# Kernel tuning notes

Hardware: AMD Instinct MI355X
Metric: run time of the kernel (lower is better)

The kernel has to match this reference:

```python
import jax, jax.numpy as jnp
import numpy as np

D_MODEL = 1024
NUM_HEADS = 16
D_K = D_MODEL // NUM_HEADS


def setup_inputs() -> dict:
    key = jax.random.key(0)
    ks = jax.random.split(key, 9)
    B, S = 2, 2048
    s_in = 1.0 / np.sqrt(D_MODEL)
    x = jax.random.normal(ks[0], (B, S, D_MODEL), dtype=jnp.float32)
    # Linear weights stored as (in_features, out_features): y = x @ W + b
    Wq = jax.random.uniform(ks[1], (D_MODEL, D_MODEL), jnp.float32, -s_in, s_in)
    bq = jax.random.uniform(ks[2], (D_MODEL,), jnp.float32, -s_in, s_in)
    Wk = jax.random.uniform(ks[3], (D_MODEL, D_K), jnp.float32, -s_in, s_in)
    bk = jax.random.uniform(ks[4], (D_K,), jnp.float32, -s_in, s_in)
    Wv = jax.random.uniform(ks[5], (D_MODEL, D_K), jnp.float32, -s_in, s_in)
    bv = jax.random.uniform(ks[6], (D_K,), jnp.float32, -s_in, s_in)
    Wo = jax.random.uniform(ks[7], (D_MODEL, D_MODEL), jnp.float32, -s_in, s_in)
    bo = jax.random.uniform(ks[8], (D_MODEL,), jnp.float32, -s_in, s_in)
    return {"x": x, "Wq": Wq, "bq": bq, "Wk": Wk, "bk": bk,
            "Wv": Wv, "bv": bv, "Wo": Wo, "bo": bo}


def reference(x, Wq, bq, Wk, bk, Wv, bv, Wo, bo):
    B, S, _ = x.shape
    H, Dk = NUM_HEADS, D_K
    # Projections
    Q = (x @ Wq + bq).reshape(B, S, H, Dk).transpose(0, 2, 1, 3)  # [B,H,S,Dk]
    K = x @ Wk + bk                                               # [B,S,Dk] single KV head
    V = x @ Wv + bv                                               # [B,S,Dk]
    # Scores: query heads broadcast against the single shared KV head
    scores = jnp.einsum('bhqd,bkd->bhqk', Q, K) / jnp.sqrt(jnp.float32(Dk))
    attn = jax.nn.softmax(scores, axis=-1)                        # [B,H,S,S]
    out = jnp.einsum('bhqk,bkd->bhqd', attn, V)                   # [B,H,S,Dk]
    out = out.transpose(0, 2, 1, 3).reshape(B, S, H * Dk)         # [B,S,d_model]
    return out @ Wo + bo
```

## Files before the change

### kernel.cpp

```cpp
#include <hip/hip_runtime.h>
#include <hip/hip_bf16.h>

typedef __attribute__((ext_vector_type(8))) short bf16x8;
typedef __attribute__((ext_vector_type(4))) float f32x4;
typedef __attribute__((ext_vector_type(16))) float f32x16;
typedef __attribute__((ext_vector_type(4))) unsigned short ushort4v;

#define QSCALE 0.1803368801111204f

__device__ __forceinline__ unsigned short f2bf(float f) {
  union { float f; unsigned int u; } x; x.f = f;
  unsigned int u = x.u;
  unsigned int r = (u + 0x7fffu + ((u >> 16) & 1u)) >> 16;
  return (unsigned short)r;
}

__device__ __forceinline__ unsigned int bfpack2(float a, float b) {
  union { __hip_bfloat162 h; unsigned int u; } c;
  c.h = __float22bfloat162_rn(make_float2(a, b));
  return c.u;
}

__global__ __launch_bounds__(256) void prep_kernel(
    const float* __restrict__ x,
    const float* __restrict__ Wq, const float* __restrict__ Wk,
    const float* __restrict__ Wv, const float* __restrict__ Wo,
    unsigned short* __restrict__ xb,
    unsigned short* __restrict__ QKVt, unsigned short* __restrict__ Wot) {
  int z = blockIdx.z;
  if (z == 4) {
    size_t base = ((size_t)(blockIdx.y * 32 + blockIdx.x)) * 4096 + threadIdx.x * 16;
#pragma unroll
    for (int c = 0; c < 4; ++c) {
      float4 v = *(const float4*)(x + base + c * 4);
      ushort4v o = { f2bf(v.x), f2bf(v.y), f2bf(v.z), f2bf(v.w) };
      *(ushort4v*)(xb + base + c * 4) = o;
    }
    return;
  }
  __shared__ float t[32][33];
  const float* src;
  unsigned short* dst;
  int C, rowoff;
  if (z == 0)      { src = Wq; dst = QKVt; C = 1024; rowoff = 0; }
  else if (z == 1) { src = Wk; dst = QKVt; C = 64;   rowoff = 1024; }
  else if (z == 2) { src = Wv; dst = QKVt; C = 64;   rowoff = 1088; }
  else             { src = Wo; dst = Wot;  C = 1024; rowoff = 0; }
  int c0 = blockIdx.x * 32, r0 = blockIdx.y * 32;
  if (c0 >= C) return;
  int tx = threadIdx.x & 31, ty = threadIdx.x >> 5;
#pragma unroll
  for (int i = 0; i < 32; i += 8)
    t[ty + i][tx] = src[(size_t)(r0 + ty + i) * C + c0 + tx];
  __syncthreads();
#pragma unroll
  for (int i = 0; i < 32; i += 8)
    dst[(size_t)(rowoff + c0 + ty + i) * 1024 + r0 + tx] = f2bf(t[tx][ty + i]);
}

template <typename OutT, bool QKVMODE>
__global__ __launch_bounds__(256) void gemm_bf16_kernel(
    const unsigned short* __restrict__ A, const unsigned short* __restrict__ Bt,
    const float* __restrict__ b0, const float* __restrict__ b1,
    const float* __restrict__ b2, OutT* __restrict__ C,
    unsigned short* __restrict__ Vt, int M, int N, int K) {
  constexpr int LS = 40;
  __shared__ unsigned short As[2][128 * LS];
  __shared__ unsigned short Bs[2][128 * LS];
  int tid = threadIdx.x;
  int wid = tid >> 6, lane = tid & 63;
  int l15 = lane & 15, quad = lane >> 4;
  int m0 = blockIdx.x * 128, n0 = blockIdx.y * 128;
  int mw = (wid >> 1) * 64, nw = (wid & 1) * 64;
  f32x4 acc[4][4];
#pragma unroll
  for (int i = 0; i < 4; i++)
#pragma unroll
    for (int j = 0; j < 4; j++)
#pragma unroll
      for (int e = 0; e < 4; ++e) acc[i][j][e] = 0.f;

  int arow = tid >> 2, akc = (tid & 3) * 8;
  const unsigned short* Ag = A + (size_t)(m0 + arow) * K + akc;
  const unsigned short* Bg = Bt + (size_t)(n0 + arow) * K + akc;
  bf16x8 ar0 = *(const bf16x8*)(Ag);
  bf16x8 ar1 = *(const bf16x8*)(Ag + (size_t)64 * K);
  bf16x8 br0 = *(const bf16x8*)(Bg);
  bf16x8 br1 = *(const bf16x8*)(Bg + (size_t)64 * K);

  for (int k0 = 0; k0 < K; k0 += 32) {
    unsigned short* Asb = As[(k0 >> 5) & 1];
    unsigned short* Bsb = Bs[(k0 >> 5) & 1];
    *(bf16x8*)(Asb + arow * LS + akc) = ar0;
    *(bf16x8*)(Asb + (arow + 64) * LS + akc) = ar1;
    *(bf16x8*)(Bsb + arow * LS + akc) = br0;
    *(bf16x8*)(Bsb + (arow + 64) * LS + akc) = br1;
    __syncthreads();
    if (k0 + 32 < K) {
      ar0 = *(const bf16x8*)(Ag + k0 + 32);
      ar1 = *(const bf16x8*)(Ag + (size_t)64 * K + k0 + 32);
      br0 = *(const bf16x8*)(Bg + k0 + 32);
      br1 = *(const bf16x8*)(Bg + (size_t)64 * K + k0 + 32);
    }
    bf16x8 af[4], bfr[4];
#pragma unroll
    for (int t = 0; t < 4; ++t)
      af[t] = *(const bf16x8*)(Asb + (mw + t * 16 + l15) * LS + quad * 8);
#pragma unroll
    for (int t = 0; t < 4; ++t)
      bfr[t] = *(const bf16x8*)(Bsb + (nw + t * 16 + l15) * LS + quad * 8);
#pragma unroll
    for (int mt = 0; mt < 4; ++mt)
#pragma unroll
      for (int nt = 0; nt < 4; ++nt)
        acc[mt][nt] = __builtin_amdgcn_mfma_f32_16x16x32_bf16(
            af[mt], bfr[nt], acc[mt][nt], 0, 0, 0);
  }
#pragma unroll
  for (int mt = 0; mt < 4; ++mt)
#pragma unroll
    for (int nt = 0; nt < 4; ++nt) {
      int col = n0 + nw + nt * 16 + l15;
      float bias, cs;
      if constexpr (QKVMODE) {
        bias = (col < 1024) ? b0[col] : ((col < 1088) ? b1[col - 1024] : b2[col - 1088]);
        cs = (col < 1024) ? QSCALE : 1.0f;
      } else {
        bias = b0[col];
        cs = 1.0f;
      }
#pragma unroll
      for (int r = 0; r < 4; ++r) {
        int row = m0 + mw + mt * 16 + quad * 4 + r;
        float v = (acc[mt][nt][r] + bias) * cs;
        if constexpr (sizeof(OutT) == 2)
          C[(size_t)row * N + col] = f2bf(v);
        else
          C[(size_t)row * N + col] = v;
        if constexpr (QKVMODE) {
          if (col >= 1088)
            Vt[((size_t)(row >> 11) * 64 + (col - 1088)) * 2048 + (row & 2047)] =
                f2bf(v);
        }
      }
    }
}

__global__ __launch_bounds__(256) void flash_attn_kernel(
    const unsigned short* __restrict__ QKV,
    const unsigned short* __restrict__ Vt,
    unsigned short* __restrict__ AO) {
  constexpr int S = 2048, LDQ = 1152;
  constexpr int PK = 72;
  __shared__ unsigned short Ks[2][64 * PK];
  __shared__ unsigned short Vs[2][64 * PK];
  int tid = threadIdx.x;
  int wid = tid >> 6, lane = tid & 63;
  int l31 = lane & 31, half = lane >> 5;
  int q0 = blockIdx.x * 128, h = blockIdx.y, b = blockIdx.z;

  const unsigned short* Qb =
      QKV + (size_t)(b * S + q0 + wid * 32 + l31) * LDQ + h * 64 + half * 8;
  bf16x8 qf[4];
#pragma unroll
  for (int f = 0; f < 4; ++f) qf[f] = *(const bf16x8*)(Qb + f * 16);

  int srow = tid >> 3, skc = (tid & 7) * 8;
  const unsigned short* Kg = QKV + ((size_t)(b * S + srow) * LDQ + 1024 + skc);
  const unsigned short* Vg = Vt + ((size_t)(b * 64 + srow) * 2048 + skc);

  f32x16 oacc[2];
#pragma unroll
  for (int r = 0; r < 16; ++r) { oacc[0][r] = 0.f; oacc[1][r] = 0.f; }
  float rsacc = 0.f;

  bf16x8 kr0 = *(const bf16x8*)(Kg);
  bf16x8 kr1 = *(const bf16x8*)(Kg + (size_t)32 * LDQ);
  bf16x8 vr0 = *(const bf16x8*)(Vg);
  bf16x8 vr1 = *(const bf16x8*)(Vg + (size_t)32 * 2048);

  for (int kb = 0; kb < S; kb += 64) {
    unsigned short* Ksb = Ks[(kb >> 6) & 1];
    unsigned short* Vsb = Vs[(kb >> 6) & 1];
    *(bf16x8*)(Ksb + srow * PK + skc) = kr0;
    *(bf16x8*)(Ksb + (srow + 32) * PK + skc) = kr1;
    *(bf16x8*)(Vsb + srow * PK + skc) = vr0;
    *(bf16x8*)(Vsb + (srow + 32) * PK + skc) = vr1;
    __syncthreads();
    if (kb + 64 < S) {
      kr0 = *(const bf16x8*)(Kg + (size_t)(kb + 64) * LDQ);
      kr1 = *(const bf16x8*)(Kg + (size_t)(kb + 96) * LDQ);
      vr0 = *(const bf16x8*)(Vg + kb + 64);
      vr1 = *(const bf16x8*)(Vg + (size_t)32 * 2048 + kb + 64);
    }

    unsigned int pk[2][8];
#pragma unroll
    for (int n2 = 0; n2 < 2; ++n2) {
      f32x16 sacc;
#pragma unroll
      for (int i = 0; i < 16; ++i) sacc[i] = 0.f;
#pragma unroll
      for (int s4 = 0; s4 < 4; ++s4) {
        bf16x8 kf = *(const bf16x8*)(Ksb + (n2 * 32 + l31) * PK + s4 * 16 + half * 8);
        sacc = __builtin_amdgcn_mfma_f32_32x32x16_bf16(kf, qf[s4], sacc, 0, 0, 0);
      }
#pragma unroll
      for (int v = 0; v < 8; ++v) {
        float p0 = __builtin_amdgcn_exp2f(sacc[2 * v]);
        float p1 = __builtin_amdgcn_exp2f(sacc[2 * v + 1]);
        rsacc += p0 + p1;
        pk[n2][v] = bfpack2(p0, p1);
      }
    }
    unsigned int other[2][8];
#pragma unroll
    for (int n2 = 0; n2 < 2; ++n2)
#pragma unroll
      for (int v = 0; v < 8; ++v) other[n2][v] = __shfl_xor(pk[n2][v], 32);

    bf16x8 pfr[4];
#pragma unroll
    for (int s = 0; s < 4; ++s) {
      int n2 = s >> 1, vb = 4 * (s & 1);
      union { bf16x8 v; unsigned int u[4]; } fr;
      fr.u[0] = half ? other[n2][vb + 2] : pk[n2][vb + 0];
      fr.u[1] = half ? other[n2][vb + 3] : pk[n2][vb + 1];
      fr.u[2] = half ? pk[n2][vb + 2]    : other[n2][vb + 0];
      fr.u[3] = half ? pk[n2][vb + 3]    : other[n2][vb + 1];
      pfr[s] = fr.v;
    }

#pragma unroll
    for (int d2 = 0; d2 < 2; ++d2)
#pragma unroll
      for (int s = 0; s < 4; ++s) {
        bf16x8 vf = *(const bf16x8*)(Vsb + (d2 * 32 + l31) * PK + s * 16 + half * 8);
        oacc[d2] = __builtin_amdgcn_mfma_f32_32x32x16_bf16(vf, pfr[s], oacc[d2], 0, 0, 0);
      }
  }

  float inv = 1.0f / (rsacc + __shfl_xor(rsacc, 32));

  unsigned short* Ob = AO + (size_t)(b * S + q0 + wid * 32 + l31) * 1024 + h * 64;
#pragma unroll
  for (int d2 = 0; d2 < 2; ++d2)
#pragma unroll
    for (int g = 0; g < 4; ++g) {
      union { ushort4v s4; unsigned int u[2]; } w;
      w.u[0] = bfpack2(oacc[d2][4 * g + 0] * inv, oacc[d2][4 * g + 1] * inv);
      w.u[1] = bfpack2(oacc[d2][4 * g + 2] * inv, oacc[d2][4 * g + 3] * inv);
      *(ushort4v*)(Ob + d2 * 32 + 8 * g + 4 * half) = w.s4;
    }
}

extern "C" void kernel_launch(void* const* d_in, const int* in_sizes, int n_in,
                              void* d_out, int out_size, void* d_ws, size_t ws_size,
                              hipStream_t stream) {
  const float* x  = (const float*)d_in[0];
  const float* Wq = (const float*)d_in[1];
  const float* bq = (const float*)d_in[2];
  const float* Wk = (const float*)d_in[3];
  const float* bk = (const float*)d_in[4];
  const float* Wv = (const float*)d_in[5];
  const float* bv = (const float*)d_in[6];
  const float* Wo = (const float*)d_in[7];
  const float* bo = (const float*)d_in[8];
  float* out = (float*)d_out;

  constexpr int B = 2, S = 2048, D = 1024, Dk = 64, H = 16;
  constexpr int M = B * S;
  constexpr int NQKV = D + 2 * Dk;

  char* ws = (char*)d_ws;
  unsigned short* xb   = (unsigned short*)ws; ws += (size_t)M * D * 2;
  unsigned short* QKVt = (unsigned short*)ws; ws += (size_t)NQKV * D * 2;
  unsigned short* Wot  = (unsigned short*)ws; ws += (size_t)D * D * 2;
  unsigned short* QKV  = (unsigned short*)ws; ws += (size_t)M * NQKV * 2;
  unsigned short* Vtb  = (unsigned short*)ws; ws += (size_t)B * Dk * S * 2;
  unsigned short* AO   = (unsigned short*)ws; ws += (size_t)M * D * 2;

  prep_kernel<<<dim3(32, 32, 5), 256, 0, stream>>>(x, Wq, Wk, Wv, Wo, xb, QKVt, Wot);

  gemm_bf16_kernel<unsigned short, true><<<dim3(M / 128, NQKV / 128), 256, 0, stream>>>(
      xb, QKVt, bq, bk, bv, QKV, Vtb, M, NQKV, D);

  flash_attn_kernel<<<dim3(S / 128, H, B), 256, 0, stream>>>(QKV, Vtb, AO);

  gemm_bf16_kernel<float, false><<<dim3(M / 128, D / 128), 256, 0, stream>>>(
      AO, Wot, bo, nullptr, nullptr, out, nullptr, M, D, D);
}
```

Before: 194.3 us.

## Shrink GEMM N-tile to 64 and rework attention around 16x16 MFMA tiles

The GEMM kernel now uses 128x64 tiles instead of 128x128, which doubles the number of blocks for the QKV and output projections and raises parallelism across CUs. The attention kernel is rewritten to give each wave 16 query rows using 16x16x32 MFMA instead of 32x32x16. The P fragments are now rearranged with ds_bpermute, and the launch bound now requests 4 blocks per CU. This is meant to improve occupancy and load balance, since the old grids had few blocks. In exchange, the smaller tiles lower per-block data reuse and add more redundant K/V loads into LDS.

```diff
diff --git a/kernel.cpp b/kernel.cpp
--- a/kernel.cpp
+++ b/kernel.cpp
@@ -3,7 +3,6 @@
 
 typedef __attribute__((ext_vector_type(8))) short bf16x8;
 typedef __attribute__((ext_vector_type(4))) float f32x4;
-typedef __attribute__((ext_vector_type(16))) float f32x16;
 typedef __attribute__((ext_vector_type(4))) unsigned short ushort4v;
 
 #define QSCALE 0.1803368801111204f
@@ -15,8 +14,8 @@
   return (unsigned short)r;
 }
 
-__device__ __forceinline__ unsigned int bfpack2(float a, float b) {
-  union { __hip_bfloat162 h; unsigned int u; } c;
+__device__ __forceinline__ int bfpack2(float a, float b) {
+  union { __hip_bfloat162 h; int u; } c;
   c.h = __float22bfloat162_rn(make_float2(a, b));
   return c.u;
 }
@@ -66,27 +65,26 @@
     unsigned short* __restrict__ Vt, int M, int N, int K) {
   constexpr int LS = 40;
   __shared__ unsigned short As[2][128 * LS];
-  __shared__ unsigned short Bs[2][128 * LS];
+  __shared__ unsigned short Bs[2][64 * LS];
   int tid = threadIdx.x;
   int wid = tid >> 6, lane = tid & 63;
   int l15 = lane & 15, quad = lane >> 4;
-  int m0 = blockIdx.x * 128, n0 = blockIdx.y * 128;
-  int mw = (wid >> 1) * 64, nw = (wid & 1) * 64;
-  f32x4 acc[4][4];
+  int m0 = blockIdx.x * 128, n0 = blockIdx.y * 64;
+  int mw = (wid >> 1) * 64, nw = (wid & 1) * 32;
+  f32x4 acc[4][2];
 #pragma unroll
   for (int i = 0; i < 4; i++)
 #pragma unroll
-    for (int j = 0; j < 4; j++)
+    for (int j = 0; j < 2; j++)
 #pragma unroll
       for (int e = 0; e < 4; ++e) acc[i][j][e] = 0.f;
 
   int arow = tid >> 2, akc = (tid & 3) * 8;
   const unsigned short* Ag = A + (size_t)(m0 + arow) * K + akc;
-  const unsigned short* Bg = Bt + (size_t)(n0 + arow) * K + akc;
+  const unsigned short* Bg = Bt + (size_t)(n0 + (tid >> 2)) * K + akc;
   bf16x8 ar0 = *(const bf16x8*)(Ag);
   bf16x8 ar1 = *(const bf16x8*)(Ag + (size_t)64 * K);
   bf16x8 br0 = *(const bf16x8*)(Bg);
-  bf16x8 br1 = *(const bf16x8*)(Bg + (size_t)64 * K);
 
   for (int k0 = 0; k0 < K; k0 += 32) {
     unsigned short* Asb = As[(k0 >> 5) & 1];
@@ -94,32 +92,30 @@
     *(bf16x8*)(Asb + arow * LS + akc) = ar0;
     *(bf16x8*)(Asb + (arow + 64) * LS + akc) = ar1;
     *(bf16x8*)(Bsb + arow * LS + akc) = br0;
-    *(bf16x8*)(Bsb + (arow + 64) * LS + akc) = br1;
     __syncthreads();
     if (k0 + 32 < K) {
       ar0 = *(const bf16x8*)(Ag + k0 + 32);
       ar1 = *(const bf16x8*)(Ag + (size_t)64 * K + k0 + 32);
       br0 = *(const bf16x8*)(Bg + k0 + 32);
-      br1 = *(const bf16x8*)(Bg + (size_t)64 * K + k0 + 32);
-    }
-    bf16x8 af[4], bfr[4];
+    }
+    bf16x8 af[4], bfr[2];
 #pragma unroll
     for (int t = 0; t < 4; ++t)
       af[t] = *(const bf16x8*)(Asb + (mw + t * 16 + l15) * LS + quad * 8);
 #pragma unroll
-    for (int t = 0; t < 4; ++t)
+    for (int t = 0; t < 2; ++t)
       bfr[t] = *(const bf16x8*)(Bsb + (nw + t * 16 + l15) * LS + quad * 8);
 #pragma unroll
     for (int mt = 0; mt < 4; ++mt)
 #pragma unroll
-      for (int nt = 0; nt < 4; ++nt)
+      for (int nt = 0; nt < 2; ++nt)
         acc[mt][nt] = __builtin_amdgcn_mfma_f32_16x16x32_bf16(
             af[mt], bfr[nt], acc[mt][nt], 0, 0, 0);
   }
 #pragma unroll
   for (int mt = 0; mt < 4; ++mt)
 #pragma unroll
-    for (int nt = 0; nt < 4; ++nt) {
+    for (int nt = 0; nt < 2; ++nt) {
       int col = n0 + nw + nt * 16 + l15;
       float bias, cs;
       if constexpr (QKVMODE) {
@@ -146,7 +142,7 @@
     }
 }
 
-__global__ __launch_bounds__(256) void flash_attn_kernel(
+__global__ __launch_bounds__(256, 4) void flash_attn_kernel(
     const unsigned short* __restrict__ QKV,
     const unsigned short* __restrict__ Vt,
     unsigned short* __restrict__ AO) {
@@ -156,22 +152,28 @@
   __shared__ unsigned short Vs[2][64 * PK];
   int tid = threadIdx.x;
   int wid = tid >> 6, lane = tid & 63;
-  int l31 = lane & 31, half = lane >> 5;
-  int q0 = blockIdx.x * 128, h = blockIdx.y, b = blockIdx.z;
+  int l15 = lane & 15, quad = lane >> 4;
+  int q0 = blockIdx.x * 64, h = blockIdx.y, b = blockIdx.z;
 
   const unsigned short* Qb =
-      QKV + (size_t)(b * S + q0 + wid * 32 + l31) * LDQ + h * 64 + half * 8;
-  bf16x8 qf[4];
-#pragma unroll
-  for (int f = 0; f < 4; ++f) qf[f] = *(const bf16x8*)(Qb + f * 16);
+      QKV + (size_t)(b * S + q0 + wid * 16 + l15) * LDQ + h * 64 + quad * 8;
+  bf16x8 qf[2];
+  qf[0] = *(const bf16x8*)(Qb);
+  qf[1] = *(const bf16x8*)(Qb + 32);
 
   int srow = tid >> 3, skc = (tid & 7) * 8;
   const unsigned short* Kg = QKV + ((size_t)(b * S + srow) * LDQ + 1024 + skc);
   const unsigned short* Vg = Vt + ((size_t)(b * 64 + srow) * 2048 + skc);
 
-  f32x16 oacc[2];
-#pragma unroll
-  for (int r = 0; r < 16; ++r) { oacc[0][r] = 0.f; oacc[1][r] = 0.f; }
+  int addrA = ((((quad << 1)) & 3) * 16 + l15) << 2;
+  int addrB = ((((quad << 1) + 1) & 3) * 16 + l15) << 2;
+  bool hi = quad >= 2;
+
+  f32x4 oacc[4];
+#pragma unroll
+  for (int i = 0; i < 4; ++i)
+#pragma unroll
+    for (int e = 0; e < 4; ++e) oacc[i][e] = 0.f;
   float rsacc = 0.f;
 
   bf16x8 kr0 = *(const bf16x8*)(Kg);
@@ -194,64 +196,69 @@
       vr1 = *(const bf16x8*)(Vg + (size_t)32 * 2048 + kb + 64);
     }
 
-    unsigned int pk[2][8];
-#pragma unroll
-    for (int n2 = 0; n2 < 2; ++n2) {
-      f32x16 sacc;
-#pragma unroll
-      for (int i = 0; i < 16; ++i) sacc[i] = 0.f;
-#pragma unroll
-      for (int s4 = 0; s4 < 4; ++s4) {
-        bf16x8 kf = *(const bf16x8*)(Ksb + (n2 * 32 + l31) * PK + s4 * 16 + half * 8);
-        sacc = __builtin_amdgcn_mfma_f32_32x32x16_bf16(kf, qf[s4], sacc, 0, 0, 0);
-      }
-#pragma unroll
-      for (int v = 0; v < 8; ++v) {
-        float p0 = __builtin_amdgcn_exp2f(sacc[2 * v]);
-        float p1 = __builtin_amdgcn_exp2f(sacc[2 * v + 1]);
-        rsacc += p0 + p1;
-        pk[n2][v] = bfpack2(p0, p1);
-      }
-    }
-    unsigned int other[2][8];
-#pragma unroll
-    for (int n2 = 0; n2 < 2; ++n2)
-#pragma unroll
-      for (int v = 0; v < 8; ++v) other[n2][v] = __shfl_xor(pk[n2][v], 32);
-
-    bf16x8 pfr[4];
-#pragma unroll
-    for (int s = 0; s < 4; ++s) {
-      int n2 = s >> 1, vb = 4 * (s & 1);
-      union { bf16x8 v; unsigned int u[4]; } fr;
-      fr.u[0] = half ? other[n2][vb + 2] : pk[n2][vb + 0];
-      fr.u[1] = half ? other[n2][vb + 3] : pk[n2][vb + 1];
-      fr.u[2] = half ? pk[n2][vb + 2]    : other[n2][vb + 0];
-      fr.u[3] = half ? pk[n2][vb + 3]    : other[n2][vb + 1];
-      pfr[s] = fr.v;
-    }
-
-#pragma unroll
-    for (int d2 = 0; d2 < 2; ++d2)
-#pragma unroll
-      for (int s = 0; s < 4; ++s) {
-        bf16x8 vf = *(const bf16x8*)(Vsb + (d2 * 32 + l31) * PK + s * 16 + half * 8);
-        oacc[d2] = __builtin_amdgcn_mfma_f32_32x32x16_bf16(vf, pfr[s], oacc[d2], 0, 0, 0);
-      }
-  }
-
-  float inv = 1.0f / (rsacc + __shfl_xor(rsacc, 32));
-
-  unsigned short* Ob = AO + (size_t)(b * S + q0 + wid * 32 + l31) * 1024 + h * 64;
-#pragma unroll
-  for (int d2 = 0; d2 < 2; ++d2)
-#pragma unroll
-    for (int g = 0; g < 4; ++g) {
-      union { ushort4v s4; unsigned int u[2]; } w;
-      w.u[0] = bfpack2(oacc[d2][4 * g + 0] * inv, oacc[d2][4 * g + 1] * inv);
-      w.u[1] = bfpack2(oacc[d2][4 * g + 2] * inv, oacc[d2][4 * g + 3] * inv);
-      *(ushort4v*)(Ob + d2 * 32 + 8 * g + 4 * half) = w.s4;
-    }
+    f32x4 sacc[4];
+#pragma unroll
+    for (int mt = 0; mt < 4; ++mt)
+#pragma unroll
+      for (int e = 0; e < 4; ++e) sacc[mt][e] = 0.f;
+#pragma unroll
+    for (int mt = 0; mt < 4; ++mt)
+#pragma unroll
+      for (int c = 0; c < 2; ++c) {
+        bf16x8 kf =
+            *(const bf16x8*)(Ksb + (mt * 16 + l15) * PK + c * 32 + quad * 8);
+        sacc[mt] = __builtin_amdgcn_mfma_f32_16x16x32_bf16(kf, qf[c], sacc[mt], 0, 0, 0);
+      }
+
+    int held[4][2];
+#pragma unroll
+    for (int mt = 0; mt < 4; ++mt) {
+      float p0 = __builtin_amdgcn_exp2f(sacc[mt][0]);
+      float p1 = __builtin_amdgcn_exp2f(sacc[mt][1]);
+      float p2 = __builtin_amdgcn_exp2f(sacc[mt][2]);
+      float p3 = __builtin_amdgcn_exp2f(sacc[mt][3]);
+      rsacc += (p0 + p1) + (p2 + p3);
+      held[mt][0] = bfpack2(p0, p1);
+      held[mt][1] = bfpack2(p2, p3);
+    }
+
+    bf16x8 pfr[2];
+#pragma unroll
+    for (int c = 0; c < 2; ++c) {
+      union { bf16x8 v; int u[4]; } fr;
+#pragma unroll
+      for (int d2 = 0; d2 < 4; ++d2) {
+        int a = (d2 & 2) ? addrB : addrA;
+        int t0 = __builtin_amdgcn_ds_bpermute(a, held[2 * c][d2 & 1]);
+        int t1 = __builtin_amdgcn_ds_bpermute(a, held[2 * c + 1][d2 & 1]);
+        fr.u[d2] = hi ? t1 : t0;
+      }
+      pfr[c] = fr.v;
+    }
+
+#pragma unroll
+    for (int mt2 = 0; mt2 < 4; ++mt2)
+#pragma unroll
+      for (int c = 0; c < 2; ++c) {
+        bf16x8 vf =
+            *(const bf16x8*)(Vsb + (mt2 * 16 + l15) * PK + c * 32 + quad * 8);
+        oacc[mt2] = __builtin_amdgcn_mfma_f32_16x16x32_bf16(vf, pfr[c], oacc[mt2], 0, 0, 0);
+      }
+  }
+
+  float s = rsacc;
+  s += __shfl_xor(s, 16);
+  s += __shfl_xor(s, 32);
+  float inv = 1.0f / s;
+
+  unsigned short* Ob = AO + (size_t)(b * S + q0 + wid * 16 + l15) * 1024 + h * 64;
+#pragma unroll
+  for (int mt2 = 0; mt2 < 4; ++mt2) {
+    union { ushort4v s4; int u[2]; } w;
+    w.u[0] = bfpack2(oacc[mt2][0] * inv, oacc[mt2][1] * inv);
+    w.u[1] = bfpack2(oacc[mt2][2] * inv, oacc[mt2][3] * inv);
+    *(ushort4v*)(Ob + mt2 * 16 + quad * 4) = w.s4;
+  }
 }
 
 extern "C" void kernel_launch(void* const* d_in, const int* in_sizes, int n_in,
@@ -282,11 +289,11 @@
 
   prep_kernel<<<dim3(32, 32, 5), 256, 0, stream>>>(x, Wq, Wk, Wv, Wo, xb, QKVt, Wot);
 
-  gemm_bf16_kernel<unsigned short, true><<<dim3(M / 128, NQKV / 128), 256, 0, stream>>>(
+  gemm_bf16_kernel<unsigned short, true><<<dim3(M / 128, NQKV / 64), 256, 0, stream>>>(
       xb, QKVt, bq, bk, bv, QKV, Vtb, M, NQKV, D);
 
-  flash_attn_kernel<<<dim3(S / 128, H, B), 256, 0, stream>>>(QKV, Vtb, AO);
-
-  gemm_bf16_kernel<float, false><<<dim3(M / 128, D / 128), 256, 0, stream>>>(
+  flash_attn_kernel<<<dim3(S / 64, H, B), 256, 0, stream>>>(QKV, Vtb, AO);
+
+  gemm_bf16_kernel<float, false><<<dim3(M / 128, D / 64), 256, 0, stream>>>(
       AO, Wot, bo, nullptr, nullptr, out, nullptr, M, D, D);
 }
```

New measurement: 203.1 us. 1.05x slower.

## Fuse x bf16 conversion into QKV GEMM, shrink GEMM N-tile, stage P via LDS

Applied to the files above, without the earlier changes.

Drops the separate x fp32-to-bf16 pass: the QKV GEMM now loads fp32 x directly and packs it to bf16 while staging into shared memory, which removes one full read and write of the activation buffer. Both GEMMs switch to 128x64 tiles, doubling the block count for better CU occupancy at the cost of less data reuse per block. The attention kernel now writes the P matrix to a per-wave LDS buffer and reads it back as the MFMA operand, replacing the cross-lane shuffles and selects. That adds LDS traffic and a write-then-read dependency on shared memory.

```diff
diff --git a/kernel.cpp b/kernel.cpp
--- a/kernel.cpp
+++ b/kernel.cpp
@@ -15,30 +15,27 @@
   return (unsigned short)r;
 }
 
-__device__ __forceinline__ unsigned int bfpack2(float a, float b) {
-  union { __hip_bfloat162 h; unsigned int u; } c;
+__device__ __forceinline__ int bfpack2(float a, float b) {
+  union { __hip_bfloat162 h; int u; } c;
   c.h = __float22bfloat162_rn(make_float2(a, b));
   return c.u;
 }
 
+__device__ __forceinline__ bf16x8 pack8(float4 a, float4 b) {
+  union { bf16x8 v; int u[4]; } c;
+  c.u[0] = bfpack2(a.x, a.y);
+  c.u[1] = bfpack2(a.z, a.w);
+  c.u[2] = bfpack2(b.x, b.y);
+  c.u[3] = bfpack2(b.z, b.w);
+  return c.v;
+}
+
 __global__ __launch_bounds__(256) void prep_kernel(
-    const float* __restrict__ x,
     const float* __restrict__ Wq, const float* __restrict__ Wk,
     const float* __restrict__ Wv, const float* __restrict__ Wo,
-    unsigned short* __restrict__ xb,
     unsigned short* __restrict__ QKVt, unsigned short* __restrict__ Wot) {
+  __shared__ float t[32][33];
   int z = blockIdx.z;
-  if (z == 4) {
-    size_t base = ((size_t)(blockIdx.y * 32 + blockIdx.x)) * 4096 + threadIdx.x * 16;
-#pragma unroll
-    for (int c = 0; c < 4; ++c) {
-      float4 v = *(const float4*)(x + base + c * 4);
-      ushort4v o = { f2bf(v.x), f2bf(v.y), f2bf(v.z), f2bf(v.w) };
-      *(ushort4v*)(xb + base + c * 4) = o;
-    }
-    return;
-  }
-  __shared__ float t[32][33];
   const float* src;
   unsigned short* dst;
   int C, rowoff;
@@ -58,68 +55,89 @@
     dst[(size_t)(rowoff + c0 + ty + i) * 1024 + r0 + tx] = f2bf(t[tx][ty + i]);
 }
 
-template <typename OutT, bool QKVMODE>
-__global__ __launch_bounds__(256) void gemm_bf16_kernel(
-    const unsigned short* __restrict__ A, const unsigned short* __restrict__ Bt,
+template <bool AFP32, typename OutT, bool QKVMODE>
+__global__ __launch_bounds__(256) void gemm_kernel(
+    const void* __restrict__ Av, const unsigned short* __restrict__ Bt,
     const float* __restrict__ b0, const float* __restrict__ b1,
     const float* __restrict__ b2, OutT* __restrict__ C,
     unsigned short* __restrict__ Vt, int M, int N, int K) {
   constexpr int LS = 40;
   __shared__ unsigned short As[2][128 * LS];
-  __shared__ unsigned short Bs[2][128 * LS];
+  __shared__ unsigned short Bs[2][64 * LS];
   int tid = threadIdx.x;
   int wid = tid >> 6, lane = tid & 63;
   int l15 = lane & 15, quad = lane >> 4;
-  int m0 = blockIdx.x * 128, n0 = blockIdx.y * 128;
-  int mw = (wid >> 1) * 64, nw = (wid & 1) * 64;
-  f32x4 acc[4][4];
+  int m0 = blockIdx.x * 128, n0 = blockIdx.y * 64;
+  int mw = (wid >> 1) * 64, nw = (wid & 1) * 32;
+  f32x4 acc[4][2];
 #pragma unroll
   for (int i = 0; i < 4; i++)
 #pragma unroll
-    for (int j = 0; j < 4; j++)
+    for (int j = 0; j < 2; j++)
 #pragma unroll
       for (int e = 0; e < 4; ++e) acc[i][j][e] = 0.f;
 
   int arow = tid >> 2, akc = (tid & 3) * 8;
-  const unsigned short* Ag = A + (size_t)(m0 + arow) * K + akc;
+  const unsigned short* Ag = nullptr;
+  const float* Agf = nullptr;
+  bf16x8 ar0, ar1;
+  float4 f0a, f0b, f1a, f1b;
+  if constexpr (AFP32) {
+    Agf = (const float*)Av + (size_t)(m0 + arow) * K + akc;
+    f0a = *(const float4*)(Agf);
+    f0b = *(const float4*)(Agf + 4);
+    f1a = *(const float4*)(Agf + (size_t)64 * K);
+    f1b = *(const float4*)(Agf + (size_t)64 * K + 4);
+  } else {
+    Ag = (const unsigned short*)Av + (size_t)(m0 + arow) * K + akc;
+    ar0 = *(const bf16x8*)(Ag);
+    ar1 = *(const bf16x8*)(Ag + (size_t)64 * K);
+  }
   const unsigned short* Bg = Bt + (size_t)(n0 + arow) * K + akc;
-  bf16x8 ar0 = *(const bf16x8*)(Ag);
-  bf16x8 ar1 = *(const bf16x8*)(Ag + (size_t)64 * K);
   bf16x8 br0 = *(const bf16x8*)(Bg);
-  bf16x8 br1 = *(const bf16x8*)(Bg + (size_t)64 * K);
 
   for (int k0 = 0; k0 < K; k0 += 32) {
     unsigned short* Asb = As[(k0 >> 5) & 1];
     unsigned short* Bsb = Bs[(k0 >> 5) & 1];
-    *(bf16x8*)(Asb + arow * LS + akc) = ar0;
-    *(bf16x8*)(Asb + (arow + 64) * LS + akc) = ar1;
+    if constexpr (AFP32) {
+      *(bf16x8*)(Asb + arow * LS + akc) = pack8(f0a, f0b);
+      *(bf16x8*)(Asb + (arow + 64) * LS + akc) = pack8(f1a, f1b);
+    } else {
+      *(bf16x8*)(Asb + arow * LS + akc) = ar0;
+      *(bf16x8*)(Asb + (arow + 64) * LS + akc) = ar1;
+    }
     *(bf16x8*)(Bsb + arow * LS + akc) = br0;
-    *(bf16x8*)(Bsb + (arow + 64) * LS + akc) = br1;
     __syncthreads();
     if (k0 + 32 < K) {
-      ar0 = *(const bf16x8*)(Ag + k0 + 32);
-      ar1 = *(const bf16x8*)(Ag + (size_t)64 * K + k0 + 32);
+      if constexpr (AFP32) {
+        f0a = *(const float4*)(Agf + k0 + 32);
+        f0b = *(const float4*)(Agf + k0 + 36);
+        f1a = *(const float4*)(Agf + (size_t)64 * K + k0 + 32);
+        f1b = *(const float4*)(Agf + (size_t)64 * K + k0 + 36);
+      } else {
+        ar0 = *(const bf16x8*)(Ag + k0 + 32);
+        ar1 = *(const bf16x8*)(Ag + (size_t)64 * K + k0 + 32);
+      }
       br0 = *(const bf16x8*)(Bg + k0 + 32);
-      br1 = *(const bf16x8*)(Bg + (size_t)64 * K + k0 + 32);
-    }
-    bf16x8 af[4], bfr[4];
+    }
+    bf16x8 af[4], bfr[2];
 #pragma unroll
     for (int t = 0; t < 4; ++t)
       af[t] = *(const bf16x8*)(Asb + (mw + t * 16 + l15) * LS + quad * 8);
 #pragma unroll
-    for (int t = 0; t < 4; ++t)
+    for (int t = 0; t < 2; ++t)
       bfr[t] = *(const bf16x8*)(Bsb + (nw + t * 16 + l15) * LS + quad * 8);
 #pragma unroll
     for (int mt = 0; mt < 4; ++mt)
 #pragma unroll
-      for (int nt = 0; nt < 4; ++nt)
+      for (int nt = 0; nt < 2; ++nt)
         acc[mt][nt] = __builtin_amdgcn_mfma_f32_16x16x32_bf16(
             af[mt], bfr[nt], acc[mt][nt], 0, 0, 0);
   }
 #pragma unroll
   for (int mt = 0; mt < 4; ++mt)
 #pragma unroll
-    for (int nt = 0; nt < 4; ++nt) {
+    for (int nt = 0; nt < 2; ++nt) {
       int col = n0 + nw + nt * 16 + l15;
       float bias, cs;
       if constexpr (QKVMODE) {
@@ -151,9 +169,10 @@
     const unsigned short* __restrict__ Vt,
     unsigned short* __restrict__ AO) {
   constexpr int S = 2048, LDQ = 1152;
-  constexpr int PK = 72;
+  constexpr int PK = 72, PP = 68;
   __shared__ unsigned short Ks[2][64 * PK];
   __shared__ unsigned short Vs[2][64 * PK];
+  __shared__ unsigned short Pt[4][32 * PP];
   int tid = threadIdx.x;
   int wid = tid >> 6, lane = tid & 63;
   int l31 = lane & 31, half = lane >> 5;
@@ -168,6 +187,7 @@
   int srow = tid >> 3, skc = (tid & 7) * 8;
   const unsigned short* Kg = QKV + ((size_t)(b * S + srow) * LDQ + 1024 + skc);
   const unsigned short* Vg = Vt + ((size_t)(b * 64 + srow) * 2048 + skc);
+  unsigned short* Ptw = Pt[wid] + l31 * PP;
 
   f32x16 oacc[2];
 #pragma unroll
@@ -194,49 +214,42 @@
       vr1 = *(const bf16x8*)(Vg + (size_t)32 * 2048 + kb + 64);
     }
 
-    unsigned int pk[2][8];
-#pragma unroll
-    for (int n2 = 0; n2 < 2; ++n2) {
+#pragma unroll
+    for (int mt2 = 0; mt2 < 2; ++mt2) {
       f32x16 sacc;
 #pragma unroll
       for (int i = 0; i < 16; ++i) sacc[i] = 0.f;
 #pragma unroll
       for (int s4 = 0; s4 < 4; ++s4) {
-        bf16x8 kf = *(const bf16x8*)(Ksb + (n2 * 32 + l31) * PK + s4 * 16 + half * 8);
+        bf16x8 kf =
+            *(const bf16x8*)(Ksb + (mt2 * 32 + l31) * PK + s4 * 16 + half * 8);
         sacc = __builtin_amdgcn_mfma_f32_32x32x16_bf16(kf, qf[s4], sacc, 0, 0, 0);
       }
 #pragma unroll
-      for (int v = 0; v < 8; ++v) {
-        float p0 = __builtin_amdgcn_exp2f(sacc[2 * v]);
-        float p1 = __builtin_amdgcn_exp2f(sacc[2 * v + 1]);
-        rsacc += p0 + p1;
-        pk[n2][v] = bfpack2(p0, p1);
-      }
-    }
-    unsigned int other[2][8];
-#pragma unroll
-    for (int n2 = 0; n2 < 2; ++n2)
-#pragma unroll
-      for (int v = 0; v < 8; ++v) other[n2][v] = __shfl_xor(pk[n2][v], 32);
-
-    bf16x8 pfr[4];
-#pragma unroll
-    for (int s = 0; s < 4; ++s) {
-      int n2 = s >> 1, vb = 4 * (s & 1);
-      union { bf16x8 v; unsigned int u[4]; } fr;
-      fr.u[0] = half ? other[n2][vb + 2] : pk[n2][vb + 0];
-      fr.u[1] = half ? other[n2][vb + 3] : pk[n2][vb + 1];
-      fr.u[2] = half ? pk[n2][vb + 2]    : other[n2][vb + 0];
-      fr.u[3] = half ? pk[n2][vb + 3]    : other[n2][vb + 1];
-      pfr[s] = fr.v;
-    }
-
+      for (int g = 0; g < 4; ++g) {
+        float p0 = __builtin_amdgcn_exp2f(sacc[4 * g + 0]);
+        float p1 = __builtin_amdgcn_exp2f(sacc[4 * g + 1]);
+        float p2 = __builtin_amdgcn_exp2f(sacc[4 * g + 2]);
+        float p3 = __builtin_amdgcn_exp2f(sacc[4 * g + 3]);
+        rsacc += (p0 + p1) + (p2 + p3);
+        int2 w;
+        w.x = bfpack2(p0, p1);
+        w.y = bfpack2(p2, p3);
+        *(int2*)(Ptw + mt2 * 32 + 8 * g + 4 * half) = w;
+      }
+    }
+
+    bf16x8 pfb[4];
+#pragma unroll
+    for (int s = 0; s < 4; ++s)
+      pfb[s] = *(const bf16x8*)(Ptw + s * 16 + half * 8);
 #pragma unroll
     for (int d2 = 0; d2 < 2; ++d2)
 #pragma unroll
       for (int s = 0; s < 4; ++s) {
-        bf16x8 vf = *(const bf16x8*)(Vsb + (d2 * 32 + l31) * PK + s * 16 + half * 8);
-        oacc[d2] = __builtin_amdgcn_mfma_f32_32x32x16_bf16(vf, pfr[s], oacc[d2], 0, 0, 0);
+        bf16x8 vf =
+            *(const bf16x8*)(Vsb + (d2 * 32 + l31) * PK + s * 16 + half * 8);
+        oacc[d2] = __builtin_amdgcn_mfma_f32_32x32x16_bf16(vf, pfb[s], oacc[d2], 0, 0, 0);
       }
   }
 
@@ -247,7 +260,7 @@
   for (int d2 = 0; d2 < 2; ++d2)
 #pragma unroll
     for (int g = 0; g < 4; ++g) {
-      union { ushort4v s4; unsigned int u[2]; } w;
+      union { ushort4v s4; int u[2]; } w;
       w.u[0] = bfpack2(oacc[d2][4 * g + 0] * inv, oacc[d2][4 * g + 1] * inv);
       w.u[1] = bfpack2(oacc[d2][4 * g + 2] * inv, oacc[d2][4 * g + 3] * inv);
       *(ushort4v*)(Ob + d2 * 32 + 8 * g + 4 * half) = w.s4;
@@ -273,20 +286,19 @@
   constexpr int NQKV = D + 2 * Dk;
 
   char* ws = (char*)d_ws;
-  unsigned short* xb   = (unsigned short*)ws; ws += (size_t)M * D * 2;
   unsigned short* QKVt = (unsigned short*)ws; ws += (size_t)NQKV * D * 2;
   unsigned short* Wot  = (unsigned short*)ws; ws += (size_t)D * D * 2;
   unsigned short* QKV  = (unsigned short*)ws; ws += (size_t)M * NQKV * 2;
   unsigned short* Vtb  = (unsigned short*)ws; ws += (size_t)B * Dk * S * 2;
   unsigned short* AO   = (unsigned short*)ws; ws += (size_t)M * D * 2;
 
-  prep_kernel<<<dim3(32, 32, 5), 256, 0, stream>>>(x, Wq, Wk, Wv, Wo, xb, QKVt, Wot);
-
-  gemm_bf16_kernel<unsigned short, true><<<dim3(M / 128, NQKV / 128), 256, 0, stream>>>(
-      xb, QKVt, bq, bk, bv, QKV, Vtb, M, NQKV, D);
+  prep_kernel<<<dim3(32, 32, 4), 256, 0, stream>>>(Wq, Wk, Wv, Wo, QKVt, Wot);
+
+  gemm_kernel<true, unsigned short, true><<<dim3(M / 128, NQKV / 64), 256, 0, stream>>>(
+      x, QKVt, bq, bk, bv, QKV, Vtb, M, NQKV, D);
 
   flash_attn_kernel<<<dim3(S / 128, H, B), 256, 0, stream>>>(QKV, Vtb, AO);
 
-  gemm_bf16_kernel<float, false><<<dim3(M / 128, D / 128), 256, 0, stream>>>(
+  gemm_kernel<false, float, false><<<dim3(M / 128, D / 64), 256, 0, stream>>>(
       AO, Wot, bo, nullptr, nullptr, out, nullptr, M, D, D);
 }
```

Measured after the change: 201.1 us. 3.5% more time.

## Split attention KV range across two wave groups and route P through LDS

Applied to the files above, without the earlier changes.

The flash attention kernel now runs 512 threads per block. Two groups of four waves each handle one half of the 2048 keys for the same 128 queries, and their partial outputs and row sums are merged through shared memory at the end. The P matrix is no longer rearranged with cross-lane shuffles; each wave writes it to a private LDS tile and reads it back as the MFMA operand, and the Q/K and P/V operand order is swapped. This raises parallelism and occupancy per block. The cost is extra LDS traffic, a second barrier per iteration, and a final reduction step.

```diff
diff --git a/kernel.cpp b/kernel.cpp
--- a/kernel.cpp
+++ b/kernel.cpp
@@ -13,12 +13,6 @@
   unsigned int u = x.u;
   unsigned int r = (u + 0x7fffu + ((u >> 16) & 1u)) >> 16;
   return (unsigned short)r;
-}
-
-__device__ __forceinline__ unsigned int bfpack2(float a, float b) {
-  union { __hip_bfloat162 h; unsigned int u; } c;
-  c.h = __float22bfloat162_rn(make_float2(a, b));
-  return c.u;
 }
 
 __global__ __launch_bounds__(256) void prep_kernel(
@@ -146,112 +140,133 @@
     }
 }
 
-__global__ __launch_bounds__(256) void flash_attn_kernel(
+__global__ __launch_bounds__(512, 4) void flash_attn_kernel(
     const unsigned short* __restrict__ QKV,
     const unsigned short* __restrict__ Vt,
     unsigned short* __restrict__ AO) {
   constexpr int S = 2048, LDQ = 1152;
-  constexpr int PK = 72;
+  constexpr int PK = 72, PP = 72;
   __shared__ unsigned short Ks[2][64 * PK];
   __shared__ unsigned short Vs[2][64 * PK];
+  __shared__ unsigned short Ps[8][32 * PP];
   int tid = threadIdx.x;
   int wid = tid >> 6, lane = tid & 63;
   int l31 = lane & 31, half = lane >> 5;
+  int p = wid & 3, ks = wid >> 2;
   int q0 = blockIdx.x * 128, h = blockIdx.y, b = blockIdx.z;
 
   const unsigned short* Qb =
-      QKV + (size_t)(b * S + q0 + wid * 32 + l31) * LDQ + h * 64 + half * 8;
+      QKV + (size_t)(b * S + q0 + p * 32 + l31) * LDQ + h * 64 + half * 8;
   bf16x8 qf[4];
 #pragma unroll
   for (int f = 0; f < 4; ++f) qf[f] = *(const bf16x8*)(Qb + f * 16);
 
-  int srow = tid >> 3, skc = (tid & 7) * 8;
-  const unsigned short* Kg = QKV + ((size_t)(b * S + srow) * LDQ + 1024 + skc);
-  const unsigned short* Vg = Vt + ((size_t)(b * 64 + srow) * 2048 + skc);
-
-  f32x16 oacc[2];
-#pragma unroll
-  for (int r = 0; r < 16; ++r) { oacc[0][r] = 0.f; oacc[1][r] = 0.f; }
-  float rsacc = 0.f;
-
-  bf16x8 kr0 = *(const bf16x8*)(Kg);
-  bf16x8 kr1 = *(const bf16x8*)(Kg + (size_t)32 * LDQ);
-  bf16x8 vr0 = *(const bf16x8*)(Vg);
-  bf16x8 vr1 = *(const bf16x8*)(Vg + (size_t)32 * 2048);
-
-  for (int kb = 0; kb < S; kb += 64) {
-    unsigned short* Ksb = Ks[(kb >> 6) & 1];
-    unsigned short* Vsb = Vs[(kb >> 6) & 1];
-    *(bf16x8*)(Ksb + srow * PK + skc) = kr0;
-    *(bf16x8*)(Ksb + (srow + 32) * PK + skc) = kr1;
-    *(bf16x8*)(Vsb + srow * PK + skc) = vr0;
-    *(bf16x8*)(Vsb + (srow + 32) * PK + skc) = vr1;
+  int u = tid & 255, sl = tid >> 8;
+  int srow = u >> 2, sc = (u & 3) * 8;
+  const unsigned short* Kgb = QKV + ((size_t)b * S) * LDQ + 1024;
+  const unsigned short* Vgb = Vt + ((size_t)(b * 64 + srow)) * 2048;
+
+  f32x4 oacc[2][4];
+  f32x16 oa0, oa1;
+#pragma unroll
+  for (int r = 0; r < 16; ++r) { oa0[r] = 0.f; oa1[r] = 0.f; }
+  float rs[16];
+#pragma unroll
+  for (int r = 0; r < 16; ++r) rs[r] = 0.f;
+
+  int kb0 = sl * 1024;
+  bf16x8 ka = *(const bf16x8*)(Kgb + (size_t)(kb0 + srow) * LDQ + sc);
+  bf16x8 kc = *(const bf16x8*)(Kgb + (size_t)(kb0 + srow) * LDQ + sc + 32);
+  bf16x8 va = *(const bf16x8*)(Vgb + kb0 + sc);
+  bf16x8 vc = *(const bf16x8*)(Vgb + kb0 + sc + 32);
+
+  unsigned short* Pw = Ps[wid];
+  unsigned short* Ksb = Ks[ks];
+  unsigned short* Vsb = Vs[ks];
+
+  for (int kt = 0; kt < 16; ++kt) {
+    *(bf16x8*)(Ks[sl] + srow * PK + sc) = ka;
+    *(bf16x8*)(Ks[sl] + srow * PK + sc + 32) = kc;
+    *(bf16x8*)(Vs[sl] + srow * PK + sc) = va;
+    *(bf16x8*)(Vs[sl] + srow * PK + sc + 32) = vc;
     __syncthreads();
-    if (kb + 64 < S) {
-      kr0 = *(const bf16x8*)(Kg + (size_t)(kb + 64) * LDQ);
-      kr1 = *(const bf16x8*)(Kg + (size_t)(kb + 96) * LDQ);
-      vr0 = *(const bf16x8*)(Vg + kb + 64);
-      vr1 = *(const bf16x8*)(Vg + (size_t)32 * 2048 + kb + 64);
-    }
-
-    unsigned int pk[2][8];
+    if (kt + 1 < 16) {
+      int kbn = sl * 1024 + (kt + 1) * 64;
+      ka = *(const bf16x8*)(Kgb + (size_t)(kbn + srow) * LDQ + sc);
+      kc = *(const bf16x8*)(Kgb + (size_t)(kbn + srow) * LDQ + sc + 32);
+      va = *(const bf16x8*)(Vgb + kbn + sc);
+      vc = *(const bf16x8*)(Vgb + kbn + sc + 32);
+    }
+
 #pragma unroll
     for (int n2 = 0; n2 < 2; ++n2) {
       f32x16 sacc;
 #pragma unroll
       for (int i = 0; i < 16; ++i) sacc[i] = 0.f;
 #pragma unroll
-      for (int s4 = 0; s4 < 4; ++s4) {
-        bf16x8 kf = *(const bf16x8*)(Ksb + (n2 * 32 + l31) * PK + s4 * 16 + half * 8);
-        sacc = __builtin_amdgcn_mfma_f32_32x32x16_bf16(kf, qf[s4], sacc, 0, 0, 0);
+      for (int s = 0; s < 4; ++s) {
+        bf16x8 kf =
+            *(const bf16x8*)(Ksb + (n2 * 32 + l31) * PK + s * 16 + half * 8);
+        sacc = __builtin_amdgcn_mfma_f32_32x32x16_bf16(qf[s], kf, sacc, 0, 0, 0);
       }
 #pragma unroll
-      for (int v = 0; v < 8; ++v) {
-        float p0 = __builtin_amdgcn_exp2f(sacc[2 * v]);
-        float p1 = __builtin_amdgcn_exp2f(sacc[2 * v + 1]);
-        rsacc += p0 + p1;
-        pk[n2][v] = bfpack2(p0, p1);
+      for (int r = 0; r < 16; ++r) {
+        float pr = __builtin_amdgcn_exp2f(sacc[r]);
+        rs[r] += pr;
+        int row = (r & 3) + 8 * (r >> 2) + 4 * half;
+        Pw[row * PP + n2 * 32 + l31] = f2bf(pr);
       }
     }
-    unsigned int other[2][8];
-#pragma unroll
-    for (int n2 = 0; n2 < 2; ++n2)
-#pragma unroll
-      for (int v = 0; v < 8; ++v) other[n2][v] = __shfl_xor(pk[n2][v], 32);
-
-    bf16x8 pfr[4];
+
+    bf16x8 pf[4];
+#pragma unroll
+    for (int s = 0; s < 4; ++s)
+      pf[s] = *(const bf16x8*)(Pw + l31 * PP + s * 16 + half * 8);
 #pragma unroll
     for (int s = 0; s < 4; ++s) {
-      int n2 = s >> 1, vb = 4 * (s & 1);
-      union { bf16x8 v; unsigned int u[4]; } fr;
-      fr.u[0] = half ? other[n2][vb + 2] : pk[n2][vb + 0];
-      fr.u[1] = half ? other[n2][vb + 3] : pk[n2][vb + 1];
-      fr.u[2] = half ? pk[n2][vb + 2]    : other[n2][vb + 0];
-      fr.u[3] = half ? pk[n2][vb + 3]    : other[n2][vb + 1];
-      pfr[s] = fr.v;
-    }
-
-#pragma unroll
-    for (int d2 = 0; d2 < 2; ++d2)
-#pragma unroll
-      for (int s = 0; s < 4; ++s) {
-        bf16x8 vf = *(const bf16x8*)(Vsb + (d2 * 32 + l31) * PK + s * 16 + half * 8);
-        oacc[d2] = __builtin_amdgcn_mfma_f32_32x32x16_bf16(vf, pfr[s], oacc[d2], 0, 0, 0);
-      }
-  }
-
-  float inv = 1.0f / (rsacc + __shfl_xor(rsacc, 32));
-
-  unsigned short* Ob = AO + (size_t)(b * S + q0 + wid * 32 + l31) * 1024 + h * 64;
-#pragma unroll
-  for (int d2 = 0; d2 < 2; ++d2)
-#pragma unroll
-    for (int g = 0; g < 4; ++g) {
-      union { ushort4v s4; unsigned int u[2]; } w;
-      w.u[0] = bfpack2(oacc[d2][4 * g + 0] * inv, oacc[d2][4 * g + 1] * inv);
-      w.u[1] = bfpack2(oacc[d2][4 * g + 2] * inv, oacc[d2][4 * g + 3] * inv);
-      *(ushort4v*)(Ob + d2 * 32 + 8 * g + 4 * half) = w.s4;
-    }
+      bf16x8 vf0 = *(const bf16x8*)(Vsb + (l31)*PK + s * 16 + half * 8);
+      bf16x8 vf1 = *(const bf16x8*)(Vsb + (32 + l31) * PK + s * 16 + half * 8);
+      oa0 = __builtin_amdgcn_mfma_f32_32x32x16_bf16(pf[s], vf0, oa0, 0, 0, 0);
+      oa1 = __builtin_amdgcn_mfma_f32_32x32x16_bf16(pf[s], vf1, oa1, 0, 0, 0);
+    }
+    __syncthreads();
+  }
+
+#pragma unroll
+  for (int r = 0; r < 16; ++r) {
+    float t = rs[r];
+    t += __shfl_xor(t, 1, 32);
+    t += __shfl_xor(t, 2, 32);
+    t += __shfl_xor(t, 4, 32);
+    t += __shfl_xor(t, 8, 32);
+    t += __shfl_xor(t, 16, 32);
+    rs[r] = t;
+  }
+
+  float* Cb = (float*)Ps;
+  if (ks == 1) {
+#pragma unroll
+    for (int r = 0; r < 16; ++r) {
+      int row = (r & 3) + 8 * (r >> 2) + 4 * half;
+      Cb[(p * 32 + row) * 65 + l31] = oa0[r];
+      Cb[(p * 32 + row) * 65 + 32 + l31] = oa1[r];
+      if (l31 == 0) Cb[(p * 32 + row) * 65 + 64] = rs[r];
+    }
+  }
+  __syncthreads();
+  if (ks == 0) {
+    unsigned short* Ob = AO + (size_t)(b * S + q0 + p * 32) * 1024 + h * 64;
+#pragma unroll
+    for (int r = 0; r < 16; ++r) {
+      int row = (r & 3) + 8 * (r >> 2) + 4 * half;
+      float p0 = Cb[(p * 32 + row) * 65 + l31];
+      float p1 = Cb[(p * 32 + row) * 65 + 32 + l31];
+      float rsu = Cb[(p * 32 + row) * 65 + 64];
+      float inv = 1.0f / (rs[r] + rsu);
+      Ob[(size_t)row * 1024 + l31] = f2bf((oa0[r] + p0) * inv);
+      Ob[(size_t)row * 1024 + 32 + l31] = f2bf((oa1[r] + p1) * inv);
+    }
+  }
 }
 
 extern "C" void kernel_launch(void* const* d_in, const int* in_sizes, int n_in,
@@ -285,7 +300,7 @@
   gemm_bf16_kernel<unsigned short, true><<<dim3(M / 128, NQKV / 128), 256, 0, stream>>>(
       xb, QKVt, bq, bk, bv, QKV, Vtb, M, NQKV, D);
 
-  flash_attn_kernel<<<dim3(S / 128, H, B), 256, 0, stream>>>(QKV, Vtb, AO);
+  flash_attn_kernel<<<dim3(S / 128, H, B), 512, 0, stream>>>(QKV, Vtb, AO);
 
   gemm_bf16_kernel<float, false><<<dim3(M / 128, D / 128), 256, 0, stream>>>(
       AO, Wot, bo, nullptr, nullptr, out, nullptr, M, D, D);
```

Result: no change. 195.8 us (+0.8%).
